# Optimization experiments

Measured on AMD Instinct MI355X. Metric: run time of the kernel, lower is better.

The kernel has to match this reference:

```python
import jax, jax.numpy as jnp
import numpy as np


def setup_inputs() -> dict:
    key = jax.random.key(0)
    kq, kk, kv = jax.random.split(key, 3)
    B, H, S, D = 4, 16, 1024, 64
    Q = jax.random.normal(kq, (B, H, S, D), dtype=jnp.float32)
    K = jax.random.normal(kk, (B, H, S, D), dtype=jnp.float32)
    V = jax.random.normal(kv, (B, H, S, D), dtype=jnp.float32)
    attn_mask = jnp.ones((B, 1, 1, S), dtype=jnp.int32)  # unused by the original forward
    return {"Q": Q, "K": K, "V": V, "attn_mask": attn_mask, "d_k": D}


def reference(Q, K, V, attn_mask, d_k):
    # scores = Q @ K^T / sqrt(d_k)   -> [B, H, S, S]
    scores = jnp.einsum("bhqd,bhkd->bhqk", Q, K) / jnp.sqrt(jnp.float32(d_k))
    # attn_mask is accepted but never applied in the original module.
    p_attn = jax.nn.softmax(scores, axis=-1)
    out = jnp.einsum("bhqk,bhkd->bhqd", p_attn, V)  # [B, H, S, D]
    return (out, p_attn)
```

## Files before the change

kernel.cpp:

```cpp
#include <hip/hip_runtime.h>
#include <hip/hip_bf16.h>

#define B_N 4
#define H_N 16
#define S_N 1024
#define D_N 64
#define NELEM (B_N * H_N * S_N * D_N)

typedef __bf16 bf16;
typedef bf16  bf16x4 __attribute__((ext_vector_type(4)));
typedef bf16  bf16x8 __attribute__((ext_vector_type(8)));
typedef float f32x4  __attribute__((ext_vector_type(4)));
typedef unsigned int u32x2 __attribute__((ext_vector_type(2)));

#define AS1 __attribute__((address_space(1)))
#define AS3 __attribute__((address_space(3)))
#define GLL16(gp, lp) __builtin_amdgcn_global_load_lds((const AS1 void*)(gp), (AS3 void*)(lp), 16, 0, 0)

__global__ __launch_bounds__(256)
void prep_qk(const float* __restrict__ Q, const float* __restrict__ K,
             bf16* __restrict__ Qb, bf16* __restrict__ Kb)
{
    int t = blockIdx.x * 256 + threadIdx.x;
    const int half = NELEM / 8;
    bool isQ = t < half;
    int tt = isQ ? t : t - half;
    int row = tt >> 3, sub = tt & 7;
    const float* src = (isQ ? Q : K) + (size_t)row * 64 + sub * 8;
    float4 f0 = *(const float4*)src;
    float4 f1 = *(const float4*)(src + 4);
    float s = isQ ? 0.125f : 1.0f;
    bf16x8 o;
    o[0] = (bf16)(f0.x * s); o[1] = (bf16)(f0.y * s);
    o[2] = (bf16)(f0.z * s); o[3] = (bf16)(f0.w * s);
    o[4] = (bf16)(f1.x * s); o[5] = (bf16)(f1.y * s);
    o[6] = (bf16)(f1.z * s); o[7] = (bf16)(f1.w * s);
    int slot = isQ ? sub : (sub ^ (row & 7));
    bf16* dst = (isQ ? Qb : Kb) + (size_t)row * 64 + slot * 8;
    *(bf16x8*)dst = o;
}

__global__ __launch_bounds__(256)
void prep_v(const float* __restrict__ V, bf16* __restrict__ Vt)
{
    int wid  = blockIdx.x * 4 + (threadIdx.x >> 6);
    int lane = threadIdx.x & 63;
    int bh = wid >> 7, chunk = wid & 127;
    const float* src = V + (size_t)bh * S_N * D_N + (size_t)chunk * 8 * 64 + lane;
    bf16x8 o;
#pragma unroll
    for (int j = 0; j < 8; ++j) o[j] = (bf16)src[j * 64];
    int slot = (chunk & 7) ^ (lane & 7);
    bf16* dst = Vt + (size_t)bh * D_N * S_N + (size_t)lane * S_N
                   + (chunk >> 3) * 64 + slot * 8;
    *(bf16x8*)dst = o;
}

__global__ __launch_bounds__(256)
void sdpa_main(const bf16* __restrict__ Qb, const bf16* __restrict__ Kb,
               const bf16* __restrict__ Vt, float* __restrict__ Og,
               float* __restrict__ Pg)
{
    __shared__ __attribute__((aligned(128))) bf16 K_lds[4096];
    __shared__ __attribute__((aligned(128))) bf16 V_lds[4096];
    __shared__ __attribute__((aligned(128))) bf16 Pt_lds[4][1024];

    const int bid = blockIdx.x;
    const int swz = (bid & 7) * 128 + (bid >> 3);
    const int bh = swz >> 4, qtile = swz & 15;

    const int tid = threadIdx.x;
    const int wave = tid >> 6, lane = tid & 63;
    const int l16 = lane & 15, lgrp = lane >> 4;
    const int swx = (l16 & 7) << 4;

    const bf16* Qp = Qb + (size_t)bh * S_N * D_N;
    const bf16* Kp = Kb + (size_t)bh * S_N * D_N;
    const bf16* Vp = Vt + (size_t)bh * D_N * S_N;
    float* Op = Og + (size_t)bh * S_N * D_N;
    float* Pp = Pg + (size_t)bh * S_N * S_N;

    const int qrow = qtile * 64 + wave * 16 + l16;
    bf16x8 aq[2];
    aq[0] = *(const bf16x8*)(Qp + (size_t)qrow * 64 + lgrp * 8);
    aq[1] = *(const bf16x8*)(Qp + (size_t)qrow * 64 + 32 + lgrp * 8);

    auto scores = [&](const bf16* base, f32x4 (&acc)[4]) {
#pragma unroll
        for (int kb = 0; kb < 4; ++kb) {
            acc[kb] = (f32x4){0.f, 0.f, 0.f, 0.f};
#pragma unroll
            for (int ds = 0; ds < 2; ++ds) {
                bf16x8 bk = *(const bf16x8*)((const char*)base
                            + (kb * 16 + l16) * 128
                            + ((ds * 64 + lgrp * 16) ^ swx));
                acc[kb] = __builtin_amdgcn_mfma_f32_16x16x32_bf16(aq[ds], bk, acc[kb], 0, 0, 0);
            }
        }
    };

    float lsum[4] = {0.f, 0.f, 0.f, 0.f};
    for (int kt = 0; kt < S_N; kt += 128) {
        __syncthreads();
        const bf16* gk = Kp + (size_t)kt * 64;
        GLL16(gk + (wave     ) * 512 + lane * 8, K_lds + (wave    ) * 512);
        GLL16(gk + (wave + 4 ) * 512 + lane * 8, K_lds + (wave + 4) * 512);
        GLL16(gk + (wave + 8 ) * 512 + lane * 8, V_lds + (wave    ) * 512);
        GLL16(gk + (wave + 12) * 512 + lane * 8, V_lds + (wave + 4) * 512);
        __syncthreads();
        f32x4 acc[4];
        scores(K_lds, acc);
#pragma unroll
        for (int kb = 0; kb < 4; ++kb)
#pragma unroll
            for (int r = 0; r < 4; ++r) lsum[r] += __expf(acc[kb][r]);
        scores(V_lds, acc);
#pragma unroll
        for (int kb = 0; kb < 4; ++kb)
#pragma unroll
            for (int r = 0; r < 4; ++r) lsum[r] += __expf(acc[kb][r]);
    }
    float rl[4];
#pragma unroll
    for (int r = 0; r < 4; ++r) {
        float s = lsum[r];
        s += __shfl_xor(s, 1, 64);
        s += __shfl_xor(s, 2, 64);
        s += __shfl_xor(s, 4, 64);
        s += __shfl_xor(s, 8, 64);
        rl[r] = 1.0f / s;
    }

    f32x4 oacc[4];
#pragma unroll
    for (int db = 0; db < 4; ++db) oacc[db] = (f32x4){0.f, 0.f, 0.f, 0.f};

    const unsigned ptoff = (unsigned)(uintptr_t)(AS3 bf16*)(&Pt_lds[wave][0]);
    const int qg = qtile * 64 + wave * 16 + l16;

    for (int kt = 0; kt < S_N; kt += 64) {
        __syncthreads();
        {
            const bf16* gk = Kp + (size_t)kt * 64;
            GLL16(gk + (wave    ) * 512 + lane * 8, K_lds + (wave    ) * 512);
            GLL16(gk + (wave + 4) * 512 + lane * 8, K_lds + (wave + 4) * 512);
            const int dr = lane >> 3, c7 = lane & 7;
            GLL16(Vp + (size_t)((wave    ) * 8 + dr) * S_N + kt + c7 * 8, V_lds + (wave    ) * 512);
            GLL16(Vp + (size_t)((wave + 4) * 8 + dr) * S_N + kt + c7 * 8, V_lds + (wave + 4) * 512);
        }
        __syncthreads();

        f32x4 acc[4];
        scores(K_lds, acc);

#pragma unroll
        for (int kb = 0; kb < 4; ++kb) {
            bf16x4 pk;
#pragma unroll
            for (int r = 0; r < 4; ++r) pk[r] = (bf16)(__expf(acc[kb][r]) * rl[r]);
            *(bf16x4*)((char*)&Pt_lds[wave][0] + (kb * 16 + l16) * 32 + lgrp * 8) = pk;
        }
        asm volatile("s_waitcnt lgkmcnt(0)" ::: "memory");

#pragma unroll
        for (int ks = 0; ks < 2; ++ks) {
            bf16x8 bv0 = *(const bf16x8*)((const char*)V_lds + (l16     ) * 128 + ((ks * 64 + lgrp * 16) ^ swx));
            bf16x8 bv1 = *(const bf16x8*)((const char*)V_lds + (16 + l16) * 128 + ((ks * 64 + lgrp * 16) ^ swx));
            bf16x8 bv2 = *(const bf16x8*)((const char*)V_lds + (32 + l16) * 128 + ((ks * 64 + lgrp * 16) ^ swx));
            bf16x8 bv3 = *(const bf16x8*)((const char*)V_lds + (48 + l16) * 128 + ((ks * 64 + lgrp * 16) ^ swx));

            u32x2 t0, t1;
            unsigned a = ptoff + ks * 1024 + lgrp * 256 + l16 * 8;
            asm volatile("ds_read_b64_tr_b16 %0, %2\n\t"
                         "ds_read_b64_tr_b16 %1, %2 offset:128"
                         : "=&v"(t0), "=&v"(t1) : "v"(a));
            asm volatile("s_waitcnt lgkmcnt(0)" ::: "memory");
            __builtin_amdgcn_sched_barrier(0);

            bf16x8 ap;
            ((unsigned*)&ap)[0] = t0[0]; ((unsigned*)&ap)[1] = t0[1];
            ((unsigned*)&ap)[2] = t1[0]; ((unsigned*)&ap)[3] = t1[1];

            float4 o0, o1;
            o0.x = __uint_as_float(t0[0] << 16);
            o0.y = __uint_as_float(t0[0] & 0xffff0000u);
            o0.z = __uint_as_float(t0[1] << 16);
            o0.w = __uint_as_float(t0[1] & 0xffff0000u);
            o1.x = __uint_as_float(t1[0] << 16);
            o1.y = __uint_as_float(t1[0] & 0xffff0000u);
            o1.z = __uint_as_float(t1[1] << 16);
            o1.w = __uint_as_float(t1[1] & 0xffff0000u);
            float* pp = Pp + (size_t)qg * S_N + kt + ks * 32 + lgrp * 8;
            *(float4*)pp = o0;
            *(float4*)(pp + 4) = o1;

            oacc[0] = __builtin_amdgcn_mfma_f32_16x16x32_bf16(ap, bv0, oacc[0], 0, 0, 0);
            oacc[1] = __builtin_amdgcn_mfma_f32_16x16x32_bf16(ap, bv1, oacc[1], 0, 0, 0);
            oacc[2] = __builtin_amdgcn_mfma_f32_16x16x32_bf16(ap, bv2, oacc[2], 0, 0, 0);
            oacc[3] = __builtin_amdgcn_mfma_f32_16x16x32_bf16(ap, bv3, oacc[3], 0, 0, 0);
        }
    }

    const int qb0 = qtile * 64 + wave * 16 + lgrp * 4;
#pragma unroll
    for (int db = 0; db < 4; ++db)
#pragma unroll
        for (int r = 0; r < 4; ++r)
            Op[(size_t)(qb0 + r) * D_N + db * 16 + l16] = oacc[db][r];
}

__global__ __launch_bounds__(256)
void sdpa_fused(const float* __restrict__ Qg, const float* __restrict__ Kg,
                const float* __restrict__ Vg, float* __restrict__ Og,
                float* __restrict__ Pg)
{
    constexpr int LDP = 72;
    __shared__ bf16 K_lds [64][LDP];
    __shared__ bf16 Vt_lds[64][LDP];
    __shared__ bf16 P_lds [4][16][LDP];

    const int qtile = blockIdx.x;
    const int bh    = blockIdx.y;
    const int tid   = threadIdx.x;
    const int wave  = tid >> 6;
    const int lane  = tid & 63;
    const int l16   = lane & 15;
    const int lgrp  = lane >> 4;

    const float* Qp = Qg + (size_t)bh * S_N * D_N;
    const float* Kp = Kg + (size_t)bh * S_N * D_N;
    const float* Vp = Vg + (size_t)bh * S_N * D_N;
    float* Op = Og + (size_t)bh * S_N * D_N;
    float* Pp = Pg + (size_t)bh * S_N * S_N;

    const int qrow = qtile * 64 + wave * 16 + l16;
    bf16x8 aq[2];
#pragma unroll
    for (int ds = 0; ds < 2; ++ds) {
        const float* src = Qp + qrow * D_N + ds * 32 + lgrp * 8;
        float4 f0 = *(const float4*)(src);
        float4 f1 = *(const float4*)(src + 4);
        aq[ds][0] = (bf16)(f0.x * 0.125f); aq[ds][1] = (bf16)(f0.y * 0.125f);
        aq[ds][2] = (bf16)(f0.z * 0.125f); aq[ds][3] = (bf16)(f0.w * 0.125f);
        aq[ds][4] = (bf16)(f1.x * 0.125f); aq[ds][5] = (bf16)(f1.y * 0.125f);
        aq[ds][6] = (bf16)(f1.z * 0.125f); aq[ds][7] = (bf16)(f1.w * 0.125f);
    }

    auto stage_k = [&](int kt) {
#pragma unroll
        for (int i = 0; i < 4; ++i) {
            int slot = tid + i * 256;
            int row = slot >> 4, c4 = slot & 15;
            float4 f = *(const float4*)(Kp + (kt + row) * D_N + c4 * 4);
            bf16x4 pk = {(bf16)f.x, (bf16)f.y, (bf16)f.z, (bf16)f.w};
            *(bf16x4*)&K_lds[row][c4 * 4] = pk;
        }
    };
    auto stage_v = [&](int kt) {
#pragma unroll
        for (int i = 0; i < 4; ++i) {
            int slot = tid + i * 256;
            int row = slot >> 4, c4 = slot & 15;
            float4 f = *(const float4*)(Vp + (kt + row) * D_N + c4 * 4);
            Vt_lds[c4 * 4 + 0][row] = (bf16)f.x;
            Vt_lds[c4 * 4 + 1][row] = (bf16)f.y;
            Vt_lds[c4 * 4 + 2][row] = (bf16)f.z;
            Vt_lds[c4 * 4 + 3][row] = (bf16)f.w;
        }
    };
    auto compute_scores = [&](f32x4 (&acc)[4]) {
#pragma unroll
        for (int kb = 0; kb < 4; ++kb) {
            acc[kb] = (f32x4){0.f, 0.f, 0.f, 0.f};
#pragma unroll
            for (int ds = 0; ds < 2; ++ds) {
                bf16x8 bk = *(const bf16x8*)&K_lds[kb * 16 + l16][ds * 32 + lgrp * 8];
                acc[kb] = __builtin_amdgcn_mfma_f32_16x16x32_bf16(aq[ds], bk, acc[kb], 0, 0, 0);
            }
        }
    };

    float lsum[4] = {0.f, 0.f, 0.f, 0.f};
    for (int kt = 0; kt < S_N; kt += 64) {
        __syncthreads();
        stage_k(kt);
        __syncthreads();
        f32x4 acc[4];
        compute_scores(acc);
#pragma unroll
        for (int kb = 0; kb < 4; ++kb)
#pragma unroll
            for (int r = 0; r < 4; ++r) lsum[r] += __expf(acc[kb][r]);
    }
    float rl[4];
#pragma unroll
    for (int r = 0; r < 4; ++r) {
        float s = lsum[r];
        s += __shfl_xor(s, 1, 64);
        s += __shfl_xor(s, 2, 64);
        s += __shfl_xor(s, 4, 64);
        s += __shfl_xor(s, 8, 64);
        rl[r] = 1.0f / s;
    }

    f32x4 oacc[4];
#pragma unroll
    for (int db = 0; db < 4; ++db) oacc[db] = (f32x4){0.f, 0.f, 0.f, 0.f};
    const int qb0 = qtile * 64 + wave * 16 + lgrp * 4;

    for (int kt = 0; kt < S_N; kt += 64) {
        __syncthreads();
        stage_k(kt);
        stage_v(kt);
        __syncthreads();

        f32x4 acc[4];
        compute_scores(acc);
#pragma unroll
        for (int kb = 0; kb < 4; ++kb) {
#pragma unroll
            for (int r = 0; r < 4; ++r) {
                float p = __expf(acc[kb][r]) * rl[r];
                Pp[(size_t)(qb0 + r) * S_N + (kt + kb * 16 + l16)] = p;
                P_lds[wave][lgrp * 4 + r][kb * 16 + l16] = (bf16)p;
            }
        }
#pragma unroll
        for (int ks = 0; ks < 2; ++ks) {
            bf16x8 ap = *(const bf16x8*)&P_lds[wave][l16][ks * 32 + lgrp * 8];
#pragma unroll
            for (int db = 0; db < 4; ++db) {
                bf16x8 bv = *(const bf16x8*)&Vt_lds[db * 16 + l16][ks * 32 + lgrp * 8];
                oacc[db] = __builtin_amdgcn_mfma_f32_16x16x32_bf16(ap, bv, oacc[db], 0, 0, 0);
            }
        }
    }

#pragma unroll
    for (int db = 0; db < 4; ++db)
#pragma unroll
        for (int r = 0; r < 4; ++r)
            Op[(size_t)(qb0 + r) * D_N + db * 16 + l16] = oacc[db][r];
}

extern "C" void kernel_launch(void* const* d_in, const int* in_sizes, int n_in,
                              void* d_out, int out_size, void* d_ws, size_t ws_size,
                              hipStream_t stream) {
    const float* Q = (const float*)d_in[0];
    const float* K = (const float*)d_in[1];
    const float* V = (const float*)d_in[2];
    float* Out = (float*)d_out;
    float* P   = (float*)d_out + (size_t)NELEM;

    const size_t need = (size_t)NELEM * 2 * 3;
    if (ws_size >= need) {
        bf16* Qb = (bf16*)d_ws;
        bf16* Kb = Qb + NELEM;
        bf16* Vt = Kb + NELEM;
        prep_qk<<<dim3(2 * NELEM / 8 / 256), dim3(256), 0, stream>>>(Q, K, Qb, Kb);
        prep_v<<<dim3(64 * 128 / 4), dim3(256), 0, stream>>>(V, Vt);
        sdpa_main<<<dim3(1024), dim3(256), 0, stream>>>(Qb, Kb, Vt, Out, P);
    } else {
        sdpa_fused<<<dim3(16, 64), dim3(256), 0, stream>>>(Q, K, V, Out, P);
    }
}
```

Baseline: 102.3 us.

## Double-buffer K and V tiles in LDS to overlap global loads with MFMA

Splits the K and V shared-memory tiles into two buffers and prefetches the next key tile with async global-to-LDS loads while the current one is computed, in both the row-sum pass and the output pass. Full __syncthreads calls are replaced by explicit vmcnt waits plus s_barrier. The aim is to hide global load latency behind compute. The cost is doubled LDS use, which can lower occupancy, and hand-counted vmcnt values that must match the number of outstanding loads, including the Q loads and the P stores.

Measured after the change: 105.1 us. 1.03x slower.

```diff
diff --git a/kernel.cpp b/kernel.cpp
--- a/kernel.cpp
+++ b/kernel.cpp
@@ -61,8 +61,8 @@
                const bf16* __restrict__ Vt, float* __restrict__ Og,
                float* __restrict__ Pg)
 {
-    __shared__ __attribute__((aligned(128))) bf16 K_lds[4096];
-    __shared__ __attribute__((aligned(128))) bf16 V_lds[4096];
+    __shared__ __attribute__((aligned(128))) bf16 K_lds[2][4096];
+    __shared__ __attribute__((aligned(128))) bf16 V_lds[2][4096];
     __shared__ __attribute__((aligned(128))) bf16 Pt_lds[4][1024];
 
     const int bid = blockIdx.x;
@@ -84,6 +84,17 @@
     bf16x8 aq[2];
     aq[0] = *(const bf16x8*)(Qp + (size_t)qrow * 64 + lgrp * 8);
     aq[1] = *(const bf16x8*)(Qp + (size_t)qrow * 64 + 32 + lgrp * 8);
+
+    auto stage_k = [&](int kt, int buf) {
+        const bf16* gk = Kp + (size_t)kt * 64;
+        GLL16(gk + (wave    ) * 512 + lane * 8, &K_lds[buf][(wave    ) * 512]);
+        GLL16(gk + (wave + 4) * 512 + lane * 8, &K_lds[buf][(wave + 4) * 512]);
+    };
+    auto stage_v = [&](int kt, int buf) {
+        const int dr = lane >> 3, c7 = lane & 7;
+        GLL16(Vp + (size_t)((wave    ) * 8 + dr) * S_N + kt + c7 * 8, &V_lds[buf][(wave    ) * 512]);
+        GLL16(Vp + (size_t)((wave + 4) * 8 + dr) * S_N + kt + c7 * 8, &V_lds[buf][(wave + 4) * 512]);
+    };
 
     auto scores = [&](const bf16* base, f32x4 (&acc)[4]) {
 #pragma unroll
@@ -100,25 +111,22 @@
     };
 
     float lsum[4] = {0.f, 0.f, 0.f, 0.f};
-    for (int kt = 0; kt < S_N; kt += 128) {
-        __syncthreads();
-        const bf16* gk = Kp + (size_t)kt * 64;
-        GLL16(gk + (wave     ) * 512 + lane * 8, K_lds + (wave    ) * 512);
-        GLL16(gk + (wave + 4 ) * 512 + lane * 8, K_lds + (wave + 4) * 512);
-        GLL16(gk + (wave + 8 ) * 512 + lane * 8, V_lds + (wave    ) * 512);
-        GLL16(gk + (wave + 12) * 512 + lane * 8, V_lds + (wave + 4) * 512);
-        __syncthreads();
+    stage_k(0, 0);
+    for (int t = 0; t < 16; ++t) {
+        if (t < 15) {
+            stage_k((t + 1) * 64, (t + 1) & 1);
+            asm volatile("s_waitcnt vmcnt(2)" ::: "memory");
+        } else {
+            asm volatile("s_waitcnt vmcnt(0)" ::: "memory");
+        }
+        __builtin_amdgcn_s_barrier();
         f32x4 acc[4];
-        scores(K_lds, acc);
+        scores(&K_lds[t & 1][0], acc);
 #pragma unroll
         for (int kb = 0; kb < 4; ++kb)
 #pragma unroll
             for (int r = 0; r < 4; ++r) lsum[r] += __expf(acc[kb][r]);
-        scores(V_lds, acc);
-#pragma unroll
-        for (int kb = 0; kb < 4; ++kb)
-#pragma unroll
-            for (int r = 0; r < 4; ++r) lsum[r] += __expf(acc[kb][r]);
+        __builtin_amdgcn_s_barrier();
     }
     float rl[4];
 #pragma unroll
@@ -138,20 +146,20 @@
     const unsigned ptoff = (unsigned)(uintptr_t)(AS3 bf16*)(&Pt_lds[wave][0]);
     const int qg = qtile * 64 + wave * 16 + l16;
 
-    for (int kt = 0; kt < S_N; kt += 64) {
-        __syncthreads();
-        {
-            const bf16* gk = Kp + (size_t)kt * 64;
-            GLL16(gk + (wave    ) * 512 + lane * 8, K_lds + (wave    ) * 512);
-            GLL16(gk + (wave + 4) * 512 + lane * 8, K_lds + (wave + 4) * 512);
-            const int dr = lane >> 3, c7 = lane & 7;
-            GLL16(Vp + (size_t)((wave    ) * 8 + dr) * S_N + kt + c7 * 8, V_lds + (wave    ) * 512);
-            GLL16(Vp + (size_t)((wave + 4) * 8 + dr) * S_N + kt + c7 * 8, V_lds + (wave + 4) * 512);
-        }
-        __syncthreads();
+    stage_k(0, 0);
+    stage_v(0, 0);
+    for (int t = 0; t < 16; ++t) {
+        const int kt = t * 64, buf = t & 1;
+        if (t < 15) {
+            stage_k(kt + 64, buf ^ 1);
+            stage_v(kt + 64, buf ^ 1);
+        }
+        if (t == 0 || t == 15) asm volatile("s_waitcnt vmcnt(4)" ::: "memory");
+        else                   asm volatile("s_waitcnt vmcnt(8)" ::: "memory");
+        __builtin_amdgcn_s_barrier();
 
         f32x4 acc[4];
-        scores(K_lds, acc);
+        scores(&K_lds[buf][0], acc);
 
 #pragma unroll
         for (int kb = 0; kb < 4; ++kb) {
@@ -162,12 +170,13 @@
         }
         asm volatile("s_waitcnt lgkmcnt(0)" ::: "memory");
 
+        const bf16* vb = &V_lds[buf][0];
 #pragma unroll
         for (int ks = 0; ks < 2; ++ks) {
-            bf16x8 bv0 = *(const bf16x8*)((const char*)V_lds + (l16     ) * 128 + ((ks * 64 + lgrp * 16) ^ swx));
-            bf16x8 bv1 = *(const bf16x8*)((const char*)V_lds + (16 + l16) * 128 + ((ks * 64 + lgrp * 16) ^ swx));
-            bf16x8 bv2 = *(const bf16x8*)((const char*)V_lds + (32 + l16) * 128 + ((ks * 64 + lgrp * 16) ^ swx));
-            bf16x8 bv3 = *(const bf16x8*)((const char*)V_lds + (48 + l16) * 128 + ((ks * 64 + lgrp * 16) ^ swx));
+            bf16x8 bv0 = *(const bf16x8*)((const char*)vb + (l16     ) * 128 + ((ks * 64 + lgrp * 16) ^ swx));
+            bf16x8 bv1 = *(const bf16x8*)((const char*)vb + (16 + l16) * 128 + ((ks * 64 + lgrp * 16) ^ swx));
+            bf16x8 bv2 = *(const bf16x8*)((const char*)vb + (32 + l16) * 128 + ((ks * 64 + lgrp * 16) ^ swx));
+            bf16x8 bv3 = *(const bf16x8*)((const char*)vb + (48 + l16) * 128 + ((ks * 64 + lgrp * 16) ^ swx));
 
             u32x2 t0, t1;
             unsigned a = ptoff + ks * 1024 + lgrp * 256 + l16 * 8;
@@ -199,6 +208,7 @@
             oacc[2] = __builtin_amdgcn_mfma_f32_16x16x32_bf16(ap, bv2, oacc[2], 0, 0, 0);
             oacc[3] = __builtin_amdgcn_mfma_f32_16x16x32_bf16(ap, bv3, oacc[3], 0, 0, 0);
         }
+        __builtin_amdgcn_s_barrier();
     }
 
     const int qb0 = qtile * 64 + wave * 16 + lgrp * 4;
```
